# Optimization experiments

Measured on AMD Instinct MI355X. Metric: run time of the kernel, lower is better.

## Reference

```python
import jax, jax.numpy as jnp
import numpy as np

N, M, K, R, D = 2048, 64, 2, 512, 1024   # seq len, chunk size, neighbours, neighbour len, model dim
H, L = 16, 1024                           # heads, layer_size
LCH = N // M                              # number of chunks l = 32
DH = L // H
SCALE = 1.0 / (D ** 0.5)                  # source scales by input dim, not head dim


def setup_inputs() -> dict:
    key = jax.random.key(0)
    ks = jax.random.split(key, 6)
    s = 0.02
    return {
        "x": jax.random.normal(ks[0], (N, D), jnp.float32),
        "neighbours": jax.random.normal(ks[1], (LCH, K, R, D), jnp.float32),
        "Wq": jax.random.normal(ks[2], (L, D), jnp.float32) * s,
        "Wk": jax.random.normal(ks[3], (L, D), jnp.float32) * s,
        "Wv": jax.random.normal(ks[4], (L, D), jnp.float32) * s,
        "Wo": jax.random.normal(ks[5], (D, L), jnp.float32) * s,
    }


def _attend(q_in, ctx, Wq, Wk, Wv, Wo):
    # q_in: (B, Q, D) queries; ctx: (B, K, R, D) retrieved neighbours.
    # Batches the per-chunk, per-neighbour Attention calls of the source in one pass,
    # then means over the K neighbour axis (reduce 'k m d -> m d', 'mean').
    B, Q = q_in.shape[0], q_in.shape[1]
    q = (q_in @ Wq.T).reshape(B, Q, H, DH)                     # (B,Q,H,DH)
    kk = (ctx @ Wk.T).reshape(B, K, R, H, DH)                  # (B,K,R,H,DH)
    vv = (ctx @ Wv.T).reshape(B, K, R, H, DH)
    scores = jnp.einsum('bqhe,bkrhe->bkhrq', q, kk) * SCALE    # (B,K,H,R,Q)
    # FAITHFUL quirk: source softmaxes over the QUERY axis (last dim of 'b k q')
    w = jax.nn.softmax(scores, axis=-1)
    o = jnp.einsum('bkhrq,bkrhe->bkqhe', w, vv).reshape(B, K, Q, L)
    z = jnp.einsum('bkql,dl->bkqd', o, Wo)                     # output projection (dropout=0)
    return z.mean(axis=1)                                      # mean over neighbours -> (B,Q,D)


def reference(x, neighbours, Wq, Wk, Wv, Wo):
    # attending_chunks: shift input left by m-1, zero-pad bottom, chunk into (l, m, d)
    att = jnp.concatenate([x[M - 1:], jnp.zeros((M - 1, D), x.dtype)], axis=0).reshape(LCH, M, D)
    # main loop over chunks u in [0, l-2] and their k neighbours, fully batched
    main = _attend(att[:LCH - 1], neighbours[:LCH - 1], Wq, Wk, Wv, Wo)   # (l-1, M, D)
    # last token attends to neighbours[-1]
    last = _attend(x[-1][None, None, :], neighbours[-1][None], Wq, Wk, Wv, Wo)  # (1,1,D)
    body = jnp.concatenate([main.reshape(-1, D), att[-1]], axis=0)        # (N, D)
    # pad top with m-1 zeros, keep first n rows
    out = jnp.concatenate([jnp.zeros((M - 1, D), x.dtype), body[:N - M + 1]], axis=0)
    out = out.at[:M - 1].set(x[:M - 1])
    out = out.at[-1].set(last[0, 0])
    return out
```

## Files before the change

kernel.cpp:

```cpp
#include <hip/hip_runtime.h>
#include <hip/hip_bf16.h>


using u16 = unsigned short;
using u32 = unsigned int;

typedef float  f32x4   __attribute__((ext_vector_type(4)));
typedef __bf16 bf16x8v __attribute__((ext_vector_type(8)));
typedef __bf16 bf16x4v __attribute__((ext_vector_type(4)));
typedef short  s16x4   __attribute__((ext_vector_type(4)));
typedef u16    u16x8   __attribute__((ext_vector_type(8)));
typedef u16    u16x4v  __attribute__((ext_vector_type(4)));

#define SCALE_LOG2E (1.4426950408889634f / 32.0f)

__device__ __forceinline__ u16 f2b(float f){ return __builtin_bit_cast(u16, (__bf16)f); }
__device__ __forceinline__ int swz(int row, int cb){ return row*128 + (cb ^ ((row & 7) << 4)); }

__device__ __forceinline__ void gl_lds16(const void* g, void* l) {
    __builtin_amdgcn_global_load_lds(
        (const __attribute__((address_space(1))) unsigned int*)(unsigned long long)g,
        (__attribute__((address_space(3))) unsigned int*)(unsigned int)(unsigned long long)l,
        16, 0, 0);
}

template<int OM>
__global__ __launch_bounds__(512, 2)
void gemm256(const u16* __restrict__ Ap, int lda,
             const u16* __restrict__ Bp, int ldb,
             void* __restrict__ Cp, void* __restrict__ Cp2,
             int M, int Kc, int nNt)
{
    __shared__ char Ls[131072];
    char* const Abase = Ls;
    char* const Bbase = Ls + 65536;

    const int tid  = threadIdx.x;
    const int lane = tid & 63, wave = tid >> 6;
    const int li = lane & 15, lg = lane >> 4;
    const int wr = wave >> 2, wc = wave & 3;

    const int nwg  = gridDim.x;
    const int lin  = blockIdx.x;
    const int lin2 = (lin & 7) * (nwg >> 3) + (lin >> 3);
    const long bm = (long)(lin2 / nNt) * 256;
    const long bn = (long)(lin2 % nNt) * 256;

    const int srow = tid >> 3;
    const int scol = ((tid & 7) ^ (srow & 7)) << 3;

    auto stageA = [&](int t, int hh) {
        char* d = Abase + (t & 1)*32768 + hh*16384 + wave*1024;
        long r0 = bm + hh*128 + srow;      if (r0 >= M) r0 = M - 1;
        long r1 = bm + hh*128 + 64 + srow; if (r1 >= M) r1 = M - 1;
        gl_lds16(Ap + r0*(long)lda + (long)t*64 + scol, d);
        gl_lds16(Ap + r1*(long)lda + (long)t*64 + scol, d + 8192);
    };
    auto stageB = [&](int t, int hh) {
        char* d = Bbase + (t & 1)*32768 + hh*16384 + wave*1024;
        long r0 = bn + hh*128 + srow;
        gl_lds16(Bp + r0*(long)ldb + (long)t*64 + scol, d);
        gl_lds16(Bp + (r0 + 64)*(long)ldb + (long)t*64 + scol, d + 8192);
    };

    const int NT = Kc >> 6;

    stageB(0, 0); stageB(0, 1); stageA(0, 0); stageA(0, 1); stageB(1, 0);
    asm volatile("s_waitcnt vmcnt(2)" ::: "memory");
    asm volatile("s_barrier" ::: "memory");

    const int swx = (li & 7) << 4;
    const int cb0 = (lg*16) ^ swx;
    const int cb1 = (64 + lg*16) ^ swx;
    const int arb = li;
    const int brb = (wc & 1)*64 + li;

    f32x4 acc[8][4] = {};
    bf16x8v a[4], b[4];

#define MFMA16(MH)                                                              \
    __builtin_amdgcn_s_setprio(1);                                              \
    _Pragma("unroll") for (int mt = 0; mt < 4; mt++)                            \
        _Pragma("unroll") for (int nt = 0; nt < 4; nt++)                        \
            acc[(MH)*4 + mt][nt] = __builtin_amdgcn_mfma_f32_16x16x32_bf16(     \
                a[mt], b[nt], acc[(MH)*4 + mt][nt], 0, 0, 0);                   \
    __builtin_amdgcn_s_setprio(0);

#define BAR_IN()  asm volatile("s_barrier" ::: "memory");                       \
                  asm volatile("s_waitcnt lgkmcnt(0)" ::: "memory");            \
                  __builtin_amdgcn_sched_barrier(0);
#define BAR_OUT() asm volatile("s_barrier" ::: "memory");

    for (int t = 0; t < NT - 1; ++t) {
        char* At = Abase + (t & 1)*32768 + wr*16384;
        char* Bt = Bbase + (t & 1)*32768 + (wc >> 1)*16384;

        #pragma unroll
        for (int mt = 0; mt < 4; mt++) a[mt] = *(const bf16x8v*)(At + (arb + mt*16)*128 + cb0);
        #pragma unroll
        for (int nt = 0; nt < 4; nt++) b[nt] = *(const bf16x8v*)(Bt + (brb + nt*16)*128 + cb0);
        stageB(t + 1, 1);
        BAR_IN(); MFMA16(0); BAR_OUT();
        #pragma unroll
        for (int mt = 0; mt < 4; mt++) a[mt] = *(const bf16x8v*)(At + (arb + 64 + mt*16)*128 + cb0);
        stageA(t + 1, 0);
        BAR_IN(); MFMA16(1); BAR_OUT();
        #pragma unroll
        for (int mt = 0; mt < 4; mt++) a[mt] = *(const bf16x8v*)(At + (arb + mt*16)*128 + cb1);
        #pragma unroll
        for (int nt = 0; nt < 4; nt++) b[nt] = *(const bf16x8v*)(Bt + (brb + nt*16)*128 + cb1);
        stageA(t + 1, 1);
        BAR_IN(); MFMA16(0); BAR_OUT();
        #pragma unroll
        for (int mt = 0; mt < 4; mt++) a[mt] = *(const bf16x8v*)(At + (arb + 64 + mt*16)*128 + cb1);
        if (t + 2 < NT) stageB(t + 2, 0);
        BAR_IN(); MFMA16(1);
        asm volatile("s_waitcnt vmcnt(2)" ::: "memory");
        BAR_OUT();
    }
    {
        const int t = NT - 1;
        char* At = Abase + (t & 1)*32768 + wr*16384;
        char* Bt = Bbase + (t & 1)*32768 + (wc >> 1)*16384;
        asm volatile("s_waitcnt vmcnt(0)" ::: "memory");
        asm volatile("s_barrier" ::: "memory");
        #pragma unroll
        for (int mt = 0; mt < 4; mt++) a[mt] = *(const bf16x8v*)(At + (arb + mt*16)*128 + cb0);
        #pragma unroll
        for (int nt = 0; nt < 4; nt++) b[nt] = *(const bf16x8v*)(Bt + (brb + nt*16)*128 + cb0);
        BAR_IN(); MFMA16(0); BAR_OUT();
        #pragma unroll
        for (int mt = 0; mt < 4; mt++) a[mt] = *(const bf16x8v*)(At + (arb + 64 + mt*16)*128 + cb0);
        BAR_IN(); MFMA16(1); BAR_OUT();
        #pragma unroll
        for (int mt = 0; mt < 4; mt++) a[mt] = *(const bf16x8v*)(At + (arb + mt*16)*128 + cb1);
        #pragma unroll
        for (int nt = 0; nt < 4; nt++) b[nt] = *(const bf16x8v*)(Bt + (brb + nt*16)*128 + cb1);
        BAR_IN(); MFMA16(0); BAR_OUT();
        #pragma unroll
        for (int mt = 0; mt < 4; mt++) a[mt] = *(const bf16x8v*)(At + (arb + 64 + mt*16)*128 + cb1);
        BAR_IN(); MFMA16(1); BAR_OUT();
    }
#undef MFMA16
#undef BAR_IN
#undef BAR_OUT

    #pragma unroll
    for (int ai = 0; ai < 8; ai++) {
        #pragma unroll
        for (int nt = 0; nt < 4; nt++) {
            f32x4 c = acc[ai][nt];
            const long row0 = bm + wr*128 + (ai >> 2)*64 + (ai & 3)*16 + lg*4;
            const long col  = bn + wc*64 + nt*16 + li;
            if (OM == 3) {
                if (col < 1024) {
                    u16* Ka = (u16*)Cp;
                    #pragma unroll
                    for (int j = 0; j < 4; j++) {
                        long rg = row0 + j;
                        if (rg < M) Ka[rg*1024 + col] = f2b(c[j]);
                    }
                } else {
                    u16* Vt = (u16*)Cp2;
                    if (row0 + 3 < M) {
                        bf16x4v w;
                        #pragma unroll
                        for (int j = 0; j < 4; j++) w[j] = (__bf16)c[j];
                        *(bf16x4v*)(Vt + (col - 1024)*32768L + row0) = w;
                    }
                }
            }
        }
    }
}

template<bool AF32, int OM>
__global__ __launch_bounds__(256)
void gemm128(const void* __restrict__ Ap, int lda,
             const u16* __restrict__ Bp, int ldb,
             void* __restrict__ Cp, void* __restrict__ Cp2,
             int M, int Kc, int row_off, int nNt)
{
    __shared__ char As[128*128];
    __shared__ char Bs[128*128];
    const int tid  = threadIdx.x;
    const int lane = tid & 63, wave = tid >> 6;
    const int li = lane & 15, lg = lane >> 4;
    const int wr = wave >> 1, wc = wave & 1;

    const int nwg  = gridDim.x;
    const int lin  = blockIdx.x;
    const int lin2 = (lin & 7) * (nwg >> 3) + (lin >> 3);
    const long bm = (long)(lin2 / nNt) * 128;
    const long bn = (long)(lin2 % nNt) * 128;

    const int grow = wave*32 + (lane >> 3);
    const int gcol = ((lane & 7) ^ (lane >> 3)) << 3;
    const int sr = tid >> 1, sc = (tid & 1) * 32;
    long arow_f = bm + sr; if (arow_f >= M) arow_f = M - 1;
    long arow_g[4];
    #pragma unroll
    for (int j = 0; j < 4; j++) {
        long r = bm + grow + j*8;
        arow_g[j] = (r < M) ? r : (M - 1);
    }

    f32x4 acc[4][4] = {};

    for (int k0 = 0; k0 < Kc; k0 += 64) {
        float4 a4[8];
        if (AF32) {
            const float4* ap = (const float4*)((const float*)Ap + arow_f*lda + k0 + sc);
            #pragma unroll
            for (int i = 0; i < 8; i++) a4[i] = ap[i];
        }
        __syncthreads();
        if (!AF32) {
            #pragma unroll
            for (int j = 0; j < 4; j++)
                gl_lds16((const u16*)Ap + arow_g[j]*(long)lda + k0 + gcol,
                         As + (wave*4 + j)*1024);
        }
        #pragma unroll
        for (int j = 0; j < 4; j++)
            gl_lds16(Bp + (bn + grow + j*8)*(long)ldb + k0 + gcol,
                     Bs + (wave*4 + j)*1024);
        if (AF32) {
            #pragma unroll
            for (int i = 0; i < 4; i++) {
                float4 f0 = a4[2*i], f1 = a4[2*i+1];
                bf16x8v w;
                w[0]=(__bf16)f0.x; w[1]=(__bf16)f0.y; w[2]=(__bf16)f0.z; w[3]=(__bf16)f0.w;
                w[4]=(__bf16)f1.x; w[5]=(__bf16)f1.y; w[6]=(__bf16)f1.z; w[7]=(__bf16)f1.w;
                *(bf16x8v*)(As + swz(sr, sc*2 + i*16)) = w;
            }
        }
        __syncthreads();
        #pragma unroll
        for (int es = 0; es < 2; es++) {
            bf16x8v af[4], bfv[4];
            #pragma unroll
            for (int mt = 0; mt < 4; mt++)
                af[mt] = *(const bf16x8v*)(As + swz(wr*64 + mt*16 + li, es*64 + lg*16));
            #pragma unroll
            for (int nt = 0; nt < 4; nt++)
                bfv[nt] = *(const bf16x8v*)(Bs + swz(wc*64 + nt*16 + li, es*64 + lg*16));
            #pragma unroll
            for (int mt = 0; mt < 4; mt++)
                #pragma unroll
                for (int nt = 0; nt < 4; nt++)
                    acc[mt][nt] = __builtin_amdgcn_mfma_f32_16x16x32_bf16(
                        af[mt], bfv[nt], acc[mt][nt], 0, 0, 0);
        }
    }

    #pragma unroll
    for (int mt = 0; mt < 4; mt++) {
        #pragma unroll
        for (int nt = 0; nt < 4; nt++) {
            f32x4 c = acc[mt][nt];
            const long row0 = bm + wr*64 + mt*16 + lg*4;
            const long col  = bn + wc*64 + nt*16 + li;
            if (OM == 0) {
                u16* C = (u16*)Cp;
                #pragma unroll
                for (int j = 0; j < 4; j++) {
                    long rg = row0 + j;
                    if (rg < M) C[rg*1024 + col] = f2b(c[j]);
                }
            } else if (OM == 2) {
                float* C = (float*)Cp;
                #pragma unroll
                for (int j = 0; j < 4; j++) {
                    long rg = row0 + j;
                    if (rg < M) C[(row_off + rg)*1024 + col] = c[j];
                }
            } else {
                if (col < 1024) {
                    u16* Ka = (u16*)Cp;
                    #pragma unroll
                    for (int j = 0; j < 4; j++) Ka[(row0 + j)*1024 + col] = f2b(c[j]);
                } else {
                    u16* Vt = (u16*)Cp2;
                    bf16x4v w;
                    #pragma unroll
                    for (int j = 0; j < 4; j++) w[j] = (__bf16)c[j];
                    *(bf16x4v*)(Vt + (col - 1024)*32768L + row0) = w;
                }
            }
        }
    }
}

__global__ __launch_bounds__(256)
void attn_kernel(const u16* __restrict__ Qa, const u16* __restrict__ Ka,
                 const u16* __restrict__ Vt, u16* __restrict__ Om)
{
    const int u = blockIdx.x, h = blockIdx.y;
    const int tid = threadIdx.x;
    const int lane = tid & 63, wave = tid >> 6;
    const int li = lane & 15, lg = lane >> 4;

    bf16x8v qf[4][2];
    #pragma unroll
    for (int qt = 0; qt < 4; qt++)
        #pragma unroll
        for (int es = 0; es < 2; es++)
            qf[qt][es] = *(const bf16x8v*)(Qa + (long)(63 + u*64 + qt*16 + li)*1024
                                              + h*64 + es*32 + lg*8);

    f32x4 acc[4][4] = {};

    for (int it = wave; it < 64; it += 4) {
        const int k = it >> 5, rsub = it & 31;
        const long kr = (long)u*1024 + k*512 + rsub*16;

        bf16x8v a0 = *(const bf16x8v*)(Ka + (kr + li)*1024 + h*64 + lg*8);
        bf16x8v a1 = *(const bf16x8v*)(Ka + (kr + li)*1024 + h*64 + 32 + lg*8);
        f32x4 s[4];
        #pragma unroll
        for (int qt = 0; qt < 4; qt++) {
            f32x4 c = {};
            c = __builtin_amdgcn_mfma_f32_16x16x32_bf16(a0, qf[qt][0], c, 0, 0, 0);
            c = __builtin_amdgcn_mfma_f32_16x16x32_bf16(a1, qf[qt][1], c, 0, 0, 0);
            s[qt] = c;
        }
        float p[4][4];
        #pragma unroll
        for (int qt = 0; qt < 4; qt++)
            #pragma unroll
            for (int j = 0; j < 4; j++)
                p[qt][j] = __builtin_amdgcn_exp2f(s[qt][j]);
        float rz[4];
        #pragma unroll
        for (int j = 0; j < 4; j++) {
            float z = p[0][j] + p[1][j] + p[2][j] + p[3][j];
            z += __shfl_xor(z, 1); z += __shfl_xor(z, 2);
            z += __shfl_xor(z, 4); z += __shfl_xor(z, 8);
            rz[j] = __builtin_amdgcn_rcpf(z);
        }
        s16x4 wf[4];
        #pragma unroll
        for (int qt = 0; qt < 4; qt++) {
            bf16x4v w;
            #pragma unroll
            for (int j = 0; j < 4; j++) w[j] = (__bf16)(p[qt][j] * rz[j]);
            wf[qt] = __builtin_bit_cast(s16x4, w);
        }
        #pragma unroll
        for (int et = 0; et < 4; et++) {
            s16x4 va = *(const s16x4*)(Vt + (long)(h*64 + et*16 + li)*32768 + kr + lg*4);
            #pragma unroll
            for (int qt = 0; qt < 4; qt++)
                acc[et][qt] = __builtin_amdgcn_mfma_f32_16x16x16bf16_1k(
                    va, wf[qt], acc[et][qt], 0, 0, 0);
        }
    }

    __shared__ float Osum[64*64];
    for (int w = 0; w < 4; w++) {
        if (wave == w) {
            #pragma unroll
            for (int et = 0; et < 4; et++)
                #pragma unroll
                for (int qt = 0; qt < 4; qt++)
                    #pragma unroll
                    for (int j = 0; j < 4; j++) {
                        int e = et*16 + lg*4 + j, q = qt*16 + li;
                        if (w == 0) Osum[e*64 + q]  = acc[et][qt][j];
                        else        Osum[e*64 + q] += acc[et][qt][j];
                    }
        }
        __syncthreads();
    }
    const int q = tid & 63, e0 = (tid >> 6) * 16;
    u16x8 o0, o1;
    #pragma unroll
    for (int i = 0; i < 8; i++) {
        o0[i] = f2b(0.5f * Osum[(e0 + i    )*64 + q]);
        o1[i] = f2b(0.5f * Osum[(e0 + 8 + i)*64 + q]);
    }
    u16* dst = Om + (long)(u*64 + q)*1024 + h*64 + e0;
    *(u16x8*)dst       = o0;
    *(u16x8*)(dst + 8) = o1;
}

__global__ __launch_bounds__(256)
void convert_w(const float* __restrict__ Wq, const float* __restrict__ Wk,
               const float* __restrict__ Wv, const float* __restrict__ Wo,
               u16* __restrict__ dst)
{
    int idx = blockIdx.x*256 + threadIdx.x;
    int w   = idx >> 18;
    int off = (idx & 262143) << 2;
    const float* src = (w == 0) ? Wq : (w == 1) ? Wk : (w == 2) ? Wv : Wo;
    float scv = (w == 0) ? SCALE_LOG2E : 1.0f;
    float4 v = *(const float4*)(src + off);
    u16x4v o = { f2b(v.x*scv), f2b(v.y*scv), f2b(v.z*scv), f2b(v.w*scv) };
    *(u16x4v*)(dst + (long)w*1048576 + off) = o;
}

__global__ __launch_bounds__(256)
void convert_a(const float* __restrict__ src, u16* __restrict__ dst, int n8)
{
    int i = blockIdx.x*256 + threadIdx.x;
    const int stride = gridDim.x*256;
    for (; i < n8; i += stride) {
        float4 f0 = ((const float4*)src)[2*i], f1 = ((const float4*)src)[2*i+1];
        u16x8 o = { f2b(f0.x), f2b(f0.y), f2b(f0.z), f2b(f0.w),
                    f2b(f1.x), f2b(f1.y), f2b(f1.z), f2b(f1.w) };
        ((u16x8*)dst)[i] = o;
    }
}

__global__ __launch_bounds__(256)
void last_kernel(const u16* __restrict__ Vt, u16* __restrict__ Om)
{
    const int row  = blockIdx.x*4 + (threadIdx.x >> 6);
    const int lane = threadIdx.x & 63;
    const u16* p = Vt + (long)row*32768 + 31*1024 + lane*16;
    float s = 0.f;
    #pragma unroll
    for (int hf = 0; hf < 2; hf++) {
        bf16x8v v = *(const bf16x8v*)(p + hf*8);
        #pragma unroll
        for (int i = 0; i < 8; i++) s += (float)v[i];
    }
    #pragma unroll
    for (int m = 1; m < 64; m <<= 1) s += __shfl_xor(s, m);
    if (lane == 0) Om[(long)1984*1024 + row] = f2b(0.5f * s);
}

__global__ __launch_bounds__(256)
void copy_head(const float* __restrict__ x, float* __restrict__ out)
{
    int i = blockIdx.x*256 + threadIdx.x;
    ((float4*)out)[i] = ((const float4*)x)[i];
}

extern "C" void kernel_launch(void* const* d_in, const int* in_sizes, int n_in,
                              void* d_out, int out_size, void* d_ws, size_t ws_size,
                              hipStream_t stream)
{
    const float* x  = (const float*)d_in[0];
    const float* nb = (const float*)d_in[1];
    const float* Wq = (const float*)d_in[2];
    const float* Wk = (const float*)d_in[3];
    const float* Wv = (const float*)d_in[4];
    const float* Wo = (const float*)d_in[5];
    float* out = (float*)d_out;
    char*  ws  = (char*)d_ws;

    if (ws_size < (size_t)144*1024*1024) return;
    const bool big = ws_size >= (size_t)212*1024*1024;
    u16* wW  = (u16*)ws;
    u16* Qa  = (u16*)(ws + (size_t) 8*1024*1024);
    u16* Om  = (u16*)(ws + (size_t)12*1024*1024);
    u16* Ka  = (u16*)(ws + (size_t)16*1024*1024);
    u16* Vt  = (u16*)(ws + (size_t)80*1024*1024);
    u16* Anb = (u16*)(ws + (size_t)144*1024*1024);
    u16* xb  = (u16*)(ws + (size_t)208*1024*1024);
    u16* wWq = wW, *wWk = wW + 1048576, *wWo = wW + 3*1048576;

    convert_w<<<dim3(4096), dim3(256), 0, stream>>>(Wq, Wk, Wv, Wo, wW);

    if (big) {
        convert_a<<<dim3(2048), dim3(256), 0, stream>>>(nb, Anb, 4194304);
        convert_a<<<dim3(512),  dim3(256), 0, stream>>>(x,  xb,  262144);
        gemm128<false, 0><<<dim3(128), dim3(256), 0, stream>>>(
            xb, 1024, wWq, 1024, Qa, nullptr, 2048, 1024, 0, 8);
        gemm256<3><<<dim3(1024), dim3(512), 0, stream>>>(
            Anb, 1024, wWk, 1024, Ka, Vt, 32768, 1024, 8);
    } else {
        gemm128<true, 0><<<dim3(128), dim3(256), 0, stream>>>(
            x, 1024, wWq, 1024, Qa, nullptr, 2048, 1024, 0, 8);
        gemm128<true, 3><<<dim3(4096), dim3(256), 0, stream>>>(
            nb, 1024, wWk, 1024, Ka, Vt, 32768, 1024, 0, 16);
    }

    attn_kernel<<<dim3(31, 16), dim3(256), 0, stream>>>(Qa, Ka, Vt, Om);
    last_kernel<<<dim3(256),    dim3(256), 0, stream>>>(Vt, Om);

    gemm128<false, 2><<<dim3(128), dim3(256), 0, stream>>>(
        Om, 1024, wWo, 1024, out, nullptr, 1985, 1024, 63, 8);
    copy_head<<<dim3(63), dim3(256), 0, stream>>>(x, out);
}
```

Measured before the change: 267.5 us.

## Restructure GEMM main loop into unrolled double-buffer pair with deeper prefetch

The bf16 MFMA GEMM main loop is unrolled by two K-tiles, so even and odd LDS buffers are addressed with constant offsets and no separate tail iteration is needed. Global-to-LDS staging is reordered so the A and B halves of the next tile are issued together. The vmcnt waits are relaxed from 2 to 4 outstanding loads, keeping more loads in flight during MFMA work. This assumes NT is even and depends on the loads completing in issue order. It also changes the barrier and wait pattern, which could stall if the counts are wrong.

```diff
diff --git a/kernel.cpp b/kernel.cpp
--- a/kernel.cpp
+++ b/kernel.cpp
@@ -64,9 +64,11 @@
     };
 
     const int NT = Kc >> 6;
-
-    stageB(0, 0); stageB(0, 1); stageA(0, 0); stageA(0, 1); stageB(1, 0);
-    asm volatile("s_waitcnt vmcnt(2)" ::: "memory");
+    const int NTH = NT >> 1;
+
+    stageA(0, 0); stageA(0, 1); stageB(0, 0); stageB(0, 1);
+    stageA(1, 0); stageB(1, 0);
+    asm volatile("s_waitcnt vmcnt(4)" ::: "memory");
     asm volatile("s_barrier" ::: "memory");
 
     const int swx = (li & 7) << 4;
@@ -90,60 +92,55 @@
                   asm volatile("s_waitcnt lgkmcnt(0)" ::: "memory");            \
                   __builtin_amdgcn_sched_barrier(0);
 #define BAR_OUT() asm volatile("s_barrier" ::: "memory");
-
-    for (int t = 0; t < NT - 1; ++t) {
-        char* At = Abase + (t & 1)*32768 + wr*16384;
-        char* Bt = Bbase + (t & 1)*32768 + (wc >> 1)*16384;
-
-        #pragma unroll
-        for (int mt = 0; mt < 4; mt++) a[mt] = *(const bf16x8v*)(At + (arb + mt*16)*128 + cb0);
-        #pragma unroll
-        for (int nt = 0; nt < 4; nt++) b[nt] = *(const bf16x8v*)(Bt + (brb + nt*16)*128 + cb0);
-        stageB(t + 1, 1);
+#define RD_A(BASE, OFS, CB)                                                     \
+    _Pragma("unroll") for (int mt = 0; mt < 4; mt++)                            \
+        a[mt] = *(const bf16x8v*)((BASE) + (arb + (OFS) + mt*16)*128 + (CB));
+#define RD_B(BASE, CB)                                                          \
+    _Pragma("unroll") for (int nt = 0; nt < 4; nt++)                            \
+        b[nt] = *(const bf16x8v*)((BASE) + (brb + nt*16)*128 + (CB));
+
+    for (int i = 0; i < NTH; ++i) {
+        const int t0 = 2*i;
+        char* Ae = Abase + wr*16384;
+        char* Be = Bbase + (wc >> 1)*16384;
+        char* Ao = Ae + 32768;
+        char* Bo = Be + 32768;
+        const bool s2 = (t0 + 2) < NT, s3 = (t0 + 3) < NT;
+
+        RD_A(Ae, 0, cb0); RD_B(Be, cb0);
+        stageA(t0 + 1, 1); stageB(t0 + 1, 1);
         BAR_IN(); MFMA16(0); BAR_OUT();
-        #pragma unroll
-        for (int mt = 0; mt < 4; mt++) a[mt] = *(const bf16x8v*)(At + (arb + 64 + mt*16)*128 + cb0);
-        stageA(t + 1, 0);
+        RD_A(Ae, 64, cb0);
         BAR_IN(); MFMA16(1); BAR_OUT();
-        #pragma unroll
-        for (int mt = 0; mt < 4; mt++) a[mt] = *(const bf16x8v*)(At + (arb + mt*16)*128 + cb1);
-        #pragma unroll
-        for (int nt = 0; nt < 4; nt++) b[nt] = *(const bf16x8v*)(Bt + (brb + nt*16)*128 + cb1);
-        stageA(t + 1, 1);
+        RD_A(Ae, 0, cb1); RD_B(Be, cb1);
         BAR_IN(); MFMA16(0); BAR_OUT();
-        #pragma unroll
-        for (int mt = 0; mt < 4; mt++) a[mt] = *(const bf16x8v*)(At + (arb + 64 + mt*16)*128 + cb1);
-        if (t + 2 < NT) stageB(t + 2, 0);
+        RD_A(Ae, 64, cb1);
+        if (s2) { stageA(t0 + 2, 0); stageB(t0 + 2, 0); }
         BAR_IN(); MFMA16(1);
-        asm volatile("s_waitcnt vmcnt(2)" ::: "memory");
+        if (s2) { asm volatile("s_waitcnt vmcnt(4)" ::: "memory"); }
+        else    { asm volatile("s_waitcnt vmcnt(0)" ::: "memory"); }
         BAR_OUT();
-    }
-    {
-        const int t = NT - 1;
-        char* At = Abase + (t & 1)*32768 + wr*16384;
-        char* Bt = Bbase + (t & 1)*32768 + (wc >> 1)*16384;
-        asm volatile("s_waitcnt vmcnt(0)" ::: "memory");
-        asm volatile("s_barrier" ::: "memory");
-        #pragma unroll
-        for (int mt = 0; mt < 4; mt++) a[mt] = *(const bf16x8v*)(At + (arb + mt*16)*128 + cb0);
-        #pragma unroll
-        for (int nt = 0; nt < 4; nt++) b[nt] = *(const bf16x8v*)(Bt + (brb + nt*16)*128 + cb0);
+        RD_A(Ao, 0, cb0); RD_B(Bo, cb0);
+        if (s2) { stageA(t0 + 2, 1); stageB(t0 + 2, 1); }
         BAR_IN(); MFMA16(0); BAR_OUT();
-        #pragma unroll
-        for (int mt = 0; mt < 4; mt++) a[mt] = *(const bf16x8v*)(At + (arb + 64 + mt*16)*128 + cb0);
+        RD_A(Ao, 64, cb0);
         BAR_IN(); MFMA16(1); BAR_OUT();
-        #pragma unroll
-        for (int mt = 0; mt < 4; mt++) a[mt] = *(const bf16x8v*)(At + (arb + mt*16)*128 + cb1);
-        #pragma unroll
-        for (int nt = 0; nt < 4; nt++) b[nt] = *(const bf16x8v*)(Bt + (brb + nt*16)*128 + cb1);
+        RD_A(Ao, 0, cb1); RD_B(Bo, cb1);
         BAR_IN(); MFMA16(0); BAR_OUT();
-        #pragma unroll
-        for (int mt = 0; mt < 4; mt++) a[mt] = *(const bf16x8v*)(At + (arb + 64 + mt*16)*128 + cb1);
-        BAR_IN(); MFMA16(1); BAR_OUT();
+        RD_A(Ao, 64, cb1);
+        if (s3) { stageA(t0 + 3, 0); stageB(t0 + 3, 0); }
+        BAR_IN(); MFMA16(1);
+        if (i + 1 < NTH) {
+            if (s3) { asm volatile("s_waitcnt vmcnt(4)" ::: "memory"); }
+            else    { asm volatile("s_waitcnt vmcnt(0)" ::: "memory"); }
+        }
+        BAR_OUT();
     }
 #undef MFMA16
 #undef BAR_IN
 #undef BAR_OUT
+#undef RD_A
+#undef RD_B
 
     #pragma unroll
     for (int ai = 0; ai < 8; ai++) {
```

After: 295.2 us. +10.4%, slower.
